# Performance work log

Measured on AMD Instinct MI355X. Metric: run time of the kernel, lower is better.

Reference implementation:

```python
import jax, jax.numpy as jnp
import numpy as np
from jax import lax

K = 3      # kernel_size
C = 64     # n_feat
B, H, W = 2, 256, 256


def _conv(x, w, b, pad):
    # NCHW conv, stride 1
    out = lax.conv_general_dilated(x, w, (1, 1), [(pad, pad), (pad, pad)],
                                   dimension_numbers=('NCHW', 'OIHW', 'NCHW'))
    return out + b[None, :, None, None]


def _prelu(x, a):
    # nn.PReLU() with a single shared learnable slope (init 0.25)
    return jnp.where(x >= 0, x, a * x)


def setup_inputs():
    key = jax.random.key(0)
    ks = jax.random.split(key, 20)
    s = 0.05
    def w(k, shape):
        return jax.random.normal(k, shape, jnp.float32) * s
    inp = {
        'image': jax.random.normal(ks[0], (B, C, H, W), jnp.float32),
        'guidance': jax.random.normal(ks[1], (B, C, H, W), jnp.float32),
        # self.tensor: 1x1 conv (2C -> C) + PReLU (shared with jbf_conv's act)
        'tensor_w': w(ks[2], (C, 2 * C, 1, 1)),
        'tensor_b': jnp.zeros((C,), jnp.float32),
        'a_jbf': jnp.full((1,), 0.25, jnp.float32),
        'kg_w1': w(ks[3], (C, C, 3, 3)), 'kg_b1': jnp.zeros((C,), jnp.float32),
        'kg_w2': w(ks[4], (C, C, 3, 3)), 'kg_b2': jnp.zeros((C,), jnp.float32),
        'kg_w3': w(ks[5], (C, C, 3, 3)), 'kg_b3': jnp.zeros((C,), jnp.float32),
        'kg_w4': w(ks[6], (C, C, 3, 3)), 'kg_b4': jnp.zeros((C,), jnp.float32),
        'kg_w5': w(ks[7], (K * K * C, C, 1, 1)),
        'kg_b5': jnp.zeros((K * K * C,), jnp.float32),
        'a_kg': jnp.full((1,), 0.25, jnp.float32),
        # jbf_conv: 3x3 C->C, PReLU (shared a_jbf), 3x3 C->C
        'jbf_w1': w(ks[8], (C, C, 3, 3)), 'jbf_b1': jnp.zeros((C,), jnp.float32),
        'jbf_w2': w(ks[9], (C, C, 3, 3)), 'jbf_b2': jnp.zeros((C,), jnp.float32),
    }
    return inp


def reference(image, guidance, tensor_w, tensor_b, a_jbf,
              kg_w1, kg_b1, kg_w2, kg_b2, kg_w3, kg_b3, kg_w4, kg_b4,
              kg_w5, kg_b5, a_kg, jbf_w1, jbf_b1, jbf_w2, jbf_b2):
    b, c, h, w = image.shape
    # fuse target+guidance features
    t = _prelu(_conv(jnp.concatenate([image, guidance], axis=1), tensor_w, tensor_b, 0), a_jbf)
    # concat_kg: predict per-pixel dynamic kernel (b, K*K*c, h, w)
    y = t
    for wt, bs in ((kg_w1, kg_b1), (kg_w2, kg_b2), (kg_w3, kg_b3), (kg_w4, kg_b4)):
        y = _prelu(_conv(y, wt, bs, 1), a_kg)
    bi_kernel = _conv(y, kg_w5, kg_b5, 0)
    # unfold: torch layout is channel-major (c, ki, kj) along dim 1
    p = (K - 1) // 2
    xp = jnp.pad(image, ((0, 0), (0, 0), (p, p), (p, p)))
    taps = [xp[:, :, i:i + h, j:j + w] for i in range(K) for j in range(K)]
    patch = jnp.stack(taps, axis=2).reshape(b, c * K * K, h, w)
    # NOTE: faithful to source -- (c*K*K) flat layout reinterpreted as (K*K, c)
    jbf = (patch * bi_kernel).reshape(b, K * K, c, h, w).sum(axis=1)
    out = _conv(_prelu(_conv(jbf, jbf_w1, jbf_b1, 1), a_jbf), jbf_w2, jbf_b2, 1)
    return out + image
```

## Files before the change

### kernel.cpp

```cpp
#include <hip/hip_runtime.h>

#define HW 65536

typedef __bf16 bf16x8 __attribute__((ext_vector_type(8)));
typedef float f32x16 __attribute__((ext_vector_type(16)));

__device__ inline unsigned short f2bf(float x) {
    union { float f; unsigned u; } v; v.f = x;
    unsigned r = v.u + 0x7FFF + ((v.u >> 16) & 1);
    return (unsigned short)(r >> 16);
}
__device__ inline float bfhi2f(unsigned u) {
    union { unsigned u; float f; } v; v.u = u & 0xffff0000u; return v.f;
}
__device__ inline float bflo2f(unsigned u) {
    union { unsigned u; float f; } v; v.u = u << 16; return v.f;
}

union FragU { uint4 u; bf16x8 v; };
__device__ inline bf16x8 ld_frag(const uint4* p) { FragU t; t.u = *p; return t.v; }

__global__ __launch_bounds__(256) void k_wprep(
    const float* __restrict__ w0, const float* __restrict__ w1,
    const float* __restrict__ w2, const float* __restrict__ w3,
    const float* __restrict__ w4, const float* __restrict__ w5,
    const float* __restrict__ w5c, const float* __restrict__ tw,
    unsigned short* __restrict__ wT)
{
    int y = blockIdx.y;
    unsigned short* o = wT + (size_t)y * 36864;
    if (y < 6) {
        const float* ws_[6] = {w0, w1, w2, w3, w4, w5};
        const float* w = ws_[y];
        for (int e = blockIdx.x * 256 + threadIdx.x; e < 36864; e += gridDim.x * 256) {
            int tap = e >> 12, oc = (e >> 6) & 63, ic = e & 63;
            int h = ic >> 5, ig = (ic >> 3) & 3, j = ic & 7;
            int dst = ((h * 2304) + (tap * 4 + ig) * 64 + oc) * 8 + j;
            o[dst] = f2bf(w[(oc * 64 + ic) * 9 + tap]);
        }
    } else if (y == 6) {
        for (int e = blockIdx.x * 256 + threadIdx.x; e < 36864; e += gridDim.x * 256)
            o[e] = f2bf(w5c[e]);
    } else {
        for (int e = blockIdx.x * 256 + threadIdx.x; e < 8192; e += gridDim.x * 256) {
            int oc = e >> 7, ic = e & 127;
            int kg = ic >> 3, j = ic & 7;
            o[((kg * 64 + oc) << 3) + j] = f2bf(tw[e]);
        }
    }
}

__global__ __launch_bounds__(256) void k_tr(
    const float* __restrict__ img, const float* __restrict__ gd,
    unsigned short* __restrict__ imgT, unsigned short* __restrict__ gdT)
{
    __shared__ float sT[64 * 66];
    int tid = threadIdx.x;
    int z = blockIdx.y;
    int b = z & 1;
    const float* src = (z >> 1) ? gd : img;
    unsigned short* dst = (z >> 1) ? gdT : imgT;
    int px0 = blockIdx.x * 64;
    size_t sbase = (size_t)b * 64 * HW + px0;

#pragma unroll
    for (int i = 0; i < 4; ++i) {
        int e = i * 256 + tid;
        int ic = e >> 4, seg = e & 15;
        float4 v = *(const float4*)(src + sbase + (size_t)ic * HW + seg * 4);
        float* p = &sT[ic * 66 + seg * 4];
        ((float2*)p)[0] = make_float2(v.x, v.y);
        ((float2*)p)[1] = make_float2(v.z, v.w);
    }
    __syncthreads();

    size_t dbase = (size_t)b * HW * 64 + (size_t)px0 * 64;
#pragma unroll
    for (int k = 0; k < 2; ++k) {
        int idx = k * 256 + tid;
        int px = idx >> 3, u = idx & 7;
        union { uint4 q; unsigned short h[8]; } o;
#pragma unroll
        for (int j = 0; j < 8; ++j)
            o.h[j] = f2bf(sT[(u * 8 + j) * 66 + px]);
        *(uint4*)(dst + dbase + (size_t)px * 64 + u * 8) = o.q;
    }
}

__global__ __launch_bounds__(256, 4) void k_fusem(
    const unsigned short* __restrict__ imgT, const unsigned short* __restrict__ gdT,
    const unsigned short* __restrict__ wTf, const float* __restrict__ bias,
    const float* __restrict__ a, unsigned short* __restrict__ out)
{
    __shared__ __align__(16) char smem[18688];
    uint4* sX = (uint4*)smem;
    float* sB = (float*)(smem + 18432);
    unsigned short* sT16 = (unsigned short*)smem;

    int tid = threadIdx.x;
    int wv = tid >> 6, lane = tid & 63;
    int half = lane >> 5, l31 = lane & 31;
    int b = blockIdx.z;
    int y0 = blockIdx.y * 8, x0 = blockIdx.x * 16;
    size_t zbase = (size_t)b * HW * 64;
    const uint4* wg = (const uint4*)wTf;

    if (tid < 64) sB[tid] = bias[tid];

    f32x16 acc[2];
#pragma unroll
    for (int i = 0; i < 2; ++i)
#pragma unroll
        for (int r = 0; r < 16; ++r) acc[i][r] = 0.f;

    auto loadX = [&](const unsigned short* src, uint4* rx) {
#pragma unroll
        for (int i = 0; i < 4; ++i) {
            int e = i * 256 + tid;
            int px = e >> 3, ig = e & 7;
            int gy = y0 + (px >> 4), gx = x0 + (px & 15);
            rx[i] = *(const uint4*)(src + zbase + ((size_t)(gy * 256 + gx)) * 64 + ig * 8);
        }
    };
    auto writeX = [&](const uint4* rx) {
#pragma unroll
        for (int i = 0; i < 4; ++i) {
            int e = i * 256 + tid;
            sX[(e >> 3) * 9 + (e & 7)] = rx[i];
        }
    };
    auto compute = [&](int h) {
#pragma unroll
        for (int c = 0; c < 4; ++c) {
            int ig = c * 2 + half;
            int kg = h * 8 + ig;
            bf16x8 a0 = ld_frag(&wg[kg * 64 + l31]);
            bf16x8 a1 = ld_frag(&wg[kg * 64 + 32 + l31]);
            int p0 = wv * 32 + l31;
            bf16x8 b0 = ld_frag(&sX[p0 * 9 + ig]);
            acc[0] = __builtin_amdgcn_mfma_f32_32x32x16_bf16(a0, b0, acc[0], 0, 0, 0);
            acc[1] = __builtin_amdgcn_mfma_f32_32x32x16_bf16(a1, b0, acc[1], 0, 0, 0);
        }
    };

    uint4 rx[4], ry[4];
    loadX(imgT, rx);
    writeX(rx);
    loadX(gdT, ry);
    __syncthreads();
    compute(0);
    __syncthreads();
    writeX(ry);
    __syncthreads();
    compute(1);

    float slope = a[0];
    __syncthreads();
    {
        int px = wv * 32 + l31;
#pragma unroll
        for (int ot = 0; ot < 2; ++ot)
#pragma unroll
            for (int q2 = 0; q2 < 4; ++q2) {
                unsigned short hw[4];
#pragma unroll
                for (int j = 0; j < 4; ++j) {
                    int r = (q2 << 2) | j;
                    int oc = ot * 32 + j + 8 * q2 + 4 * half;
                    float v = acc[ot][r] + sB[oc];
                    v = (v >= 0.f) ? v : slope * v;
                    hw[j] = f2bf(v);
                }
                int unit = ot * 4 + q2;
                int up = unit ^ (px & 7);
                uint2* p = (uint2*)&sT16[px * 64 + up * 8 + half * 4];
                *p = make_uint2((unsigned)hw[0] | ((unsigned)hw[1] << 16),
                                (unsigned)hw[2] | ((unsigned)hw[3] << 16));
            }
    }
    __syncthreads();
#pragma unroll
    for (int k = 0; k < 4; ++k) {
        int idx = k * 256 + tid;
        int row = idx >> 7, rem = idx & 127;
        int col = rem >> 3, u = rem & 7;
        int px = row * 16 + col;
        uint4 v = *(uint4*)&sT16[px * 64 + (u ^ (px & 7)) * 8];
        *(uint4*)(out + zbase + ((size_t)((y0 + row) * 256 + x0 + col)) * 64 + u * 8) = v;
    }
}

#define XU 5

template<int MODE>
__global__ __launch_bounds__(256, 4) void k_conv3m(
    const unsigned short* __restrict__ in, const unsigned short* __restrict__ wT,
    const float* __restrict__ bias, const float* __restrict__ a,
    const float* __restrict__ res, void* __restrict__ outv)
{
    __shared__ __align__(16) char smem[29312];
    uint4* sX0 = (uint4*)smem;
    uint4* sX1 = (uint4*)(smem + 14400);
    float* sB = (float*)(smem + 28800);
    unsigned short* sT16 = (unsigned short*)smem;

    int tid = threadIdx.x;
    int wv = tid >> 6, lane = tid & 63;
    int half = lane >> 5, l31 = lane & 31;
    int b = blockIdx.z;
    int y0 = blockIdx.y * 8, x0 = blockIdx.x * 16;
    const size_t zbase = (size_t)b * HW * 64;
    const uint4* wg = (const uint4*)wT;

    if (tid < 64) sB[tid] = bias[tid];

    f32x16 acc[2];
#pragma unroll
    for (int i = 0; i < 2; ++i)
#pragma unroll
        for (int r = 0; r < 16; ++r) acc[i][r] = 0.f;

    auto loadX = [&](int h, uint4* rx) {
#pragma unroll
        for (int i = 0; i < 3; ++i) {
            int e = i * 256 + tid;
            int cell = e >> 2, ig = e & 3;
            int r = cell / 18, c2 = cell - r * 18;
            int gy = y0 + r - 1, gx = x0 + c2 - 1;
            rx[i] = make_uint4(0, 0, 0, 0);
            if (e < 720 && gy >= 0 && gy < 256 && gx >= 0 && gx < 256)
                rx[i] = *(const uint4*)(in + zbase + ((size_t)(gy * 256 + gx)) * 64 + h * 32 + ig * 8);
        }
    };
    auto writeX = [&](uint4* sXd, const uint4* rx) {
#pragma unroll
        for (int i = 0; i < 3; ++i) {
            int e = i * 256 + tid;
            if (e < 720) sXd[(e >> 2) * XU + (e & 3)] = rx[i];
        }
    };
    auto compute = [&](int h, const uint4* sXp) {
#pragma unroll
        for (int tap = 0; tap < 9; ++tap) {
            int dy = tap / 3, dx = tap % 3;
#pragma unroll
            for (int c = 0; c < 2; ++c) {
                int ig = c * 2 + half;
                bf16x8 a0 = ld_frag(&wg[h * 2304 + (tap * 4 + ig) * 64 + l31]);
                bf16x8 a1 = ld_frag(&wg[h * 2304 + (tap * 4 + ig) * 64 + 32 + l31]);
                int p0 = wv * 32 + l31;
                int u0 = ((((p0 >> 4) + dy) * 18) + (p0 & 15) + dx) * XU + ig;
                bf16x8 b0 = ld_frag(&sXp[u0]);
                acc[0] = __builtin_amdgcn_mfma_f32_32x32x16_bf16(a0, b0, acc[0], 0, 0, 0);
                acc[1] = __builtin_amdgcn_mfma_f32_32x32x16_bf16(a1, b0, acc[1], 0, 0, 0);
            }
        }
    };

    uint4 rx[3];
    loadX(0, rx);
    writeX(sX0, rx);
    __syncthreads();
    loadX(1, rx);
    compute(0, sX0);
    writeX(sX1, rx);
    __syncthreads();
    compute(1, sX1);

    if (MODE == 0) {
        float slope = a[0];
        __syncthreads();
        {
            int px = wv * 32 + l31;
#pragma unroll
            for (int ot = 0; ot < 2; ++ot)
#pragma unroll
                for (int q2 = 0; q2 < 4; ++q2) {
                    unsigned short hw[4];
#pragma unroll
                    for (int j = 0; j < 4; ++j) {
                        int r = (q2 << 2) | j;
                        int oc = ot * 32 + j + 8 * q2 + 4 * half;
                        float v = acc[ot][r] + sB[oc];
                        v = (v >= 0.f) ? v : slope * v;
                        hw[j] = f2bf(v);
                    }
                    int unit = ot * 4 + q2;
                    int up = unit ^ (px & 7);
                    uint2* p = (uint2*)&sT16[px * 64 + up * 8 + half * 4];
                    *p = make_uint2((unsigned)hw[0] | ((unsigned)hw[1] << 16),
                                    (unsigned)hw[2] | ((unsigned)hw[3] << 16));
                }
        }
        __syncthreads();
        unsigned short* outT = (unsigned short*)outv;
#pragma unroll
        for (int k = 0; k < 4; ++k) {
            int idx = k * 256 + tid;
            int row = idx >> 7, rem = idx & 127;
            int col = rem >> 3, u = rem & 7;
            int px = row * 16 + col;
            uint4 v = *(uint4*)&sT16[px * 64 + (u ^ (px & 7)) * 8];
            *(uint4*)(outT + zbase + ((size_t)((y0 + row) * 256 + x0 + col)) * 64 + u * 8) = v;
        }
    } else {
        float* outF = (float*)outv;
        int p = wv * 32 + l31;
        int y = y0 + (p >> 4), x = x0 + (p & 15);
        size_t pbase = (size_t)b * 64 * HW + (size_t)y * 256 + x;
#pragma unroll
        for (int ot = 0; ot < 2; ++ot)
#pragma unroll
            for (int r = 0; r < 16; ++r) {
                int oc = ot * 32 + (r & 3) + 8 * (r >> 2) + 4 * half;
                float v = acc[ot][r] + sB[oc];
                v += res[pbase + (size_t)oc * HW];
                outF[pbase + (size_t)oc * HW] = v;
            }
    }
}

struct OffTab { unsigned v[9][32]; int chlo[9]; };
constexpr OffTab make_tab() {
    OffTab t{};
    for (int kk = 0; kk < 9; ++kk) {
        int chlo = (kk * 64) / 9;
        t.chlo[kk] = chlo;
        for (int ot = 0; ot < 2; ++ot)
            for (int r = 0; r < 16; ++r) {
                int cc0 = ot * 32 + (r & 3) + 8 * (r >> 2);
                int q0 = kk * 64 + cc0, q1 = q0 + 4;
                int o0 = (q0 / 9 - chlo) * 360 + (q0 % 9 / 3) * 40 + (q0 % 9 % 3);
                int o1 = (q1 / 9 - chlo) * 360 + (q1 % 9 / 3) * 40 + (q1 % 9 % 3);
                t.v[kk][ot * 16 + r] = (unsigned)o0 | ((unsigned)o1 << 16);
            }
    }
    return t;
}
__constant__ OffTab kOff = make_tab();

__global__ __launch_bounds__(256, 2) void k_jbfm(
    const unsigned short* __restrict__ y4, const float* __restrict__ img,
    const unsigned short* __restrict__ w5T, const float* __restrict__ b5,
    unsigned short* __restrict__ out)
{
    __shared__ __align__(16) char smem[78592];
    uint4* sY = (uint4*)smem;
    float* sB5 = (float*)(smem + 76288);
    unsigned short* sT16 = (unsigned short*)smem;

    int tid = threadIdx.x;
    int wv = tid >> 6, lane = tid & 63;
    int half = lane >> 5, l31 = lane & 31;
    int b = blockIdx.z;
    int y0 = blockIdx.y * 8, x0 = blockIdx.x * 32;
    size_t zbase = (size_t)b * HW * 64;
    size_t ibase = (size_t)b * 64 * HW;

    int p_off[3], p_dst[3];
    bool p_a[3], p_b[3], p_act[3];
#pragma unroll
    for (int i = 0; i < 3; ++i) {
        int e = i * 256 + tid;
        bool act = e < 720;
        int ch = e / 90, rem = e - ch * 90;
        int rp = rem / 10, seg = rem - rp * 10;
        int gy = y0 + rp - 1;
        int gxb = x0 - 4 + seg * 4;
        bool xok = (gxb >= 0 && gxb < 256);
        p_act[i] = act;
        p_a[i] = act && xok && gy >= 0 && gy < 256;
        p_b[i] = act && xok && (gy + 1) < 256;
        p_off[i] = ch * HW + gy * 256 + gxb;
        p_dst[i] = ch * 360 + rp * 40 + seg * 4;
    }

#pragma unroll
    for (int i = 0; i < 8; ++i) {
        int e = i * 256 + tid;
        int px = e >> 3, ig = e & 7;
        int gy = y0 + (px >> 5), gx = x0 + (px & 31);
        sY[px * 9 + ig] = *(const uint4*)(y4 + zbase + ((size_t)(gy * 256 + gx)) * 64 + ig * 8);
    }
    for (int e = tid; e < 576; e += 256) sB5[e] = b5[e];

    {
        uint4* sW50 = (uint4*)(smem + 36864);
        unsigned* sP0 = (unsigned*)(smem + 53248);
#pragma unroll
        for (int u = 0; u < 2; ++u) {
            int uu = u * 256 + tid;
            int cc = uu & 63, ig = uu >> 6;
            sW50[uu] = ((const uint4*)w5T)[cc * 8 + ig];
        }
        const float* rp0 = img + ibase;
#pragma unroll
        for (int i = 0; i < 3; ++i) {
            float4 fa = make_float4(0, 0, 0, 0), fb = make_float4(0, 0, 0, 0);
            if (p_a[i]) fa = *(const float4*)(rp0 + p_off[i]);
            if (p_b[i]) fb = *(const float4*)(rp0 + p_off[i] + 256);
            if (p_act[i]) {
                uint4 pk;
                pk.x = (unsigned)f2bf(fa.x) | ((unsigned)f2bf(fb.x) << 16);
                pk.y = (unsigned)f2bf(fa.y) | ((unsigned)f2bf(fb.y) << 16);
                pk.z = (unsigned)f2bf(fa.z) | ((unsigned)f2bf(fb.z) << 16);
                pk.w = (unsigned)f2bf(fa.w) | ((unsigned)f2bf(fb.w) << 16);
                *(uint4*)&sP0[p_dst[i]] = pk;
            }
        }
    }

    float jb[2][2][16];
#pragma unroll
    for (int i = 0; i < 2; ++i)
#pragma unroll
        for (int j = 0; j < 2; ++j)
#pragma unroll
            for (int r = 0; r < 16; ++r) jb[i][j][r] = 0.f;

    __syncthreads();

#pragma unroll 1
    for (int kk = 0; kk < 9; ++kk) {
        const int cur = kk & 1;
        const uint4* sW5c = (const uint4*)(smem + 36864 + cur * 8192);
        const unsigned* sPc = (const unsigned*)(smem + 53248 + cur * 11520);

        uint4 wpre0, wpre1;
        float4 pfa[3], pfb[3];
        if (kk < 8) {
            const int nk = kk + 1;
            const int chlo_n = kOff.chlo[nk];
            {
                int cc = tid & 63, ig = tid >> 6;
                wpre0 = ((const uint4*)w5T)[(nk * 64 + cc) * 8 + ig];
                int uu = 256 + tid;
                int cc1 = uu & 63, ig1 = uu >> 6;
                wpre1 = ((const uint4*)w5T)[(nk * 64 + cc1) * 8 + ig1];
            }
            const float* rp0 = img + ibase + (size_t)chlo_n * HW;
#pragma unroll
            for (int i = 0; i < 3; ++i) {
                pfa[i] = make_float4(0, 0, 0, 0);
                pfb[i] = make_float4(0, 0, 0, 0);
                if (p_a[i]) pfa[i] = *(const float4*)(rp0 + p_off[i]);
                if (p_b[i]) pfb[i] = *(const float4*)(rp0 + p_off[i] + 256);
            }
        }

        f32x16 acc[2][2];
#pragma unroll
        for (int ot = 0; ot < 2; ++ot)
#pragma unroll
            for (int r = 0; r < 16; ++r) {
                int cc0 = ot * 32 + (r & 3) + 8 * (r >> 2);
                float bv = sB5[kk * 64 + cc0 + 4 * half];
                acc[ot][0][r] = bv;
                acc[ot][1][r] = bv;
            }

#pragma unroll
        for (int c = 0; c < 4; ++c) {
            int ig = c * 2 + half;
            bf16x8 a0 = ld_frag(&sW5c[ig * 64 + l31]);
            bf16x8 a1 = ld_frag(&sW5c[ig * 64 + 32 + l31]);
            int p0 = wv * 64 + l31;
            bf16x8 b0 = ld_frag(&sY[p0 * 9 + ig]);
            bf16x8 b1 = ld_frag(&sY[(p0 + 32) * 9 + ig]);
            acc[0][0] = __builtin_amdgcn_mfma_f32_32x32x16_bf16(a0, b0, acc[0][0], 0, 0, 0);
            acc[0][1] = __builtin_amdgcn_mfma_f32_32x32x16_bf16(a0, b1, acc[0][1], 0, 0, 0);
            acc[1][0] = __builtin_amdgcn_mfma_f32_32x32x16_bf16(a1, b0, acc[1][0], 0, 0, 0);
            acc[1][1] = __builtin_amdgcn_mfma_f32_32x32x16_bf16(a1, b1, acc[1][1], 0, 0, 0);
        }

        {
            const unsigned* basep = sPc + wv * 80 + l31 + 3;
            const unsigned* tab = kOff.v[kk];
#pragma unroll
            for (int ot = 0; ot < 2; ++ot)
#pragma unroll
                for (int r = 0; r < 16; ++r) {
                    unsigned oo = tab[ot * 16 + r];
                    unsigned o0 = oo & 0xffffu, o1 = oo >> 16;
                    unsigned pv = basep[half ? o1 : o0];
                    jb[ot][0][r] = fmaf(acc[ot][0][r], bflo2f(pv), jb[ot][0][r]);
                    jb[ot][1][r] = fmaf(acc[ot][1][r], bfhi2f(pv), jb[ot][1][r]);
                }
        }

        if (kk < 8) {
            uint4* sW5n = (uint4*)(smem + 36864 + (cur ^ 1) * 8192);
            unsigned* sPn = (unsigned*)(smem + 53248 + (cur ^ 1) * 11520);
            sW5n[tid] = wpre0;
            sW5n[256 + tid] = wpre1;
#pragma unroll
            for (int i = 0; i < 3; ++i) {
                if (p_act[i]) {
                    uint4 pk;
                    pk.x = (unsigned)f2bf(pfa[i].x) | ((unsigned)f2bf(pfb[i].x) << 16);
                    pk.y = (unsigned)f2bf(pfa[i].y) | ((unsigned)f2bf(pfb[i].y) << 16);
                    pk.z = (unsigned)f2bf(pfa[i].z) | ((unsigned)f2bf(pfb[i].z) << 16);
                    pk.w = (unsigned)f2bf(pfa[i].w) | ((unsigned)f2bf(pfb[i].w) << 16);
                    *(uint4*)&sPn[p_dst[i]] = pk;
                }
            }
        }
        __syncthreads();
    }

#pragma unroll
    for (int ot = 0; ot < 2; ++ot)
#pragma unroll
        for (int pt = 0; pt < 2; ++pt) {
            int px = wv * 64 + pt * 32 + l31;
#pragma unroll
            for (int q2 = 0; q2 < 4; ++q2) {
                unsigned short hw[4];
#pragma unroll
                for (int j = 0; j < 4; ++j) {
                    int r = (q2 << 2) | j;
                    hw[j] = f2bf(jb[ot][pt][r]);
                }
                int unit = ot * 4 + q2;
                int up = unit ^ (px & 7);
                uint2* p = (uint2*)&sT16[px * 64 + up * 8 + half * 4];
                *p = make_uint2((unsigned)hw[0] | ((unsigned)hw[1] << 16),
                                (unsigned)hw[2] | ((unsigned)hw[3] << 16));
            }
        }
    __syncthreads();
#pragma unroll
    for (int k = 0; k < 8; ++k) {
        int col = tid >> 3, u = tid & 7;
        int px = k * 32 + col;
        uint4 v = *(uint4*)&sT16[px * 64 + (u ^ (px & 7)) * 8];
        *(uint4*)(out + zbase + ((size_t)((y0 + k) * 256 + x0 + col)) * 64 + u * 8) = v;
    }
}

extern "C" void kernel_launch(void* const* d_in, const int* in_sizes, int n_in,
                              void* d_out, int out_size, void* d_ws, size_t ws_size,
                              hipStream_t stream) {
    const float* img  = (const float*)d_in[0];
    const float* gd   = (const float*)d_in[1];
    const float* tw   = (const float*)d_in[2];
    const float* tb   = (const float*)d_in[3];
    const float* ajbf = (const float*)d_in[4];
    const float* kw1  = (const float*)d_in[5];
    const float* kb1  = (const float*)d_in[6];
    const float* kw2  = (const float*)d_in[7];
    const float* kb2  = (const float*)d_in[8];
    const float* kw3  = (const float*)d_in[9];
    const float* kb3  = (const float*)d_in[10];
    const float* kw4  = (const float*)d_in[11];
    const float* kb4  = (const float*)d_in[12];
    const float* kw5  = (const float*)d_in[13];
    const float* kb5  = (const float*)d_in[14];
    const float* akg  = (const float*)d_in[15];
    const float* jw1  = (const float*)d_in[16];
    const float* jb1  = (const float*)d_in[17];
    const float* jw2  = (const float*)d_in[18];
    const float* jb2  = (const float*)d_in[19];
    float* out  = (float*)d_out;

    const size_t TEN = (size_t)2 * HW * 64;
    unsigned short* bufA = (unsigned short*)d_ws;
    unsigned short* imgT = bufA + TEN;
    unsigned short* gdT  = imgT + TEN;
    unsigned short* wT   = gdT + TEN;
    unsigned short* bufB = (unsigned short*)d_out;

    dim3 gs(16, 32, 2);
    dim3 gw(8, 32, 2);

    k_tr<<<dim3(1024, 4), 256, 0, stream>>>(img, gd, imgT, gdT);
    k_wprep<<<dim3(4, 8), 256, 0, stream>>>(kw1, kw2, kw3, kw4, jw1, jw2, kw5, tw, wT);

    k_fusem<<<gs, 256, 0, stream>>>(imgT, gdT, wT + (size_t)7 * 36864, tb, ajbf, bufA);

    k_conv3m<0><<<gs, 256, 0, stream>>>(bufA, wT + (size_t)0 * 36864, kb1, akg, nullptr, bufB);
    k_conv3m<0><<<gs, 256, 0, stream>>>(bufB, wT + (size_t)1 * 36864, kb2, akg, nullptr, bufA);
    k_conv3m<0><<<gs, 256, 0, stream>>>(bufA, wT + (size_t)2 * 36864, kb3, akg, nullptr, bufB);
    k_conv3m<0><<<gs, 256, 0, stream>>>(bufB, wT + (size_t)3 * 36864, kb4, akg, nullptr, bufA);

    k_jbfm<<<gw, 256, 0, stream>>>(bufA, img, wT + (size_t)6 * 36864, kb5, bufB);

    k_conv3m<0><<<gs, 256, 0, stream>>>(bufB, wT + (size_t)4 * 36864, jb1, ajbf, nullptr, bufA);
    k_conv3m<2><<<gs, 256, 0, stream>>>(bufA, wT + (size_t)5 * 36864, jb2, ajbf, img, out);
}
```

Measured before the change: 313.1 us.

## Fuse consecutive 3x3 conv pairs into one kernel with halo recompute

Replaces the single 3x3 conv kernel with one that runs two chained 3x3 convs per tile. It loads a 20x12 input halo, computes the intermediate 18x10 activation into shared memory (zeroed outside the image), then runs the second conv from shared memory. This removes three kernel launches and the global round trips of the intermediate activations. In exchange it recomputes halo pixels, which adds about 40% extra MFMA work in the first conv, uses more shared memory, and splits the work unevenly because only two of the four waves handle the extra cells. The weight layout is also changed to an interleaved tap-major order.

After: 314.3 us. About the same (+0.4%).

```diff
diff --git a/kernel.cpp b/kernel.cpp
--- a/kernel.cpp
+++ b/kernel.cpp
@@ -34,8 +34,8 @@
         const float* w = ws_[y];
         for (int e = blockIdx.x * 256 + threadIdx.x; e < 36864; e += gridDim.x * 256) {
             int tap = e >> 12, oc = (e >> 6) & 63, ic = e & 63;
-            int h = ic >> 5, ig = (ic >> 3) & 3, j = ic & 7;
-            int dst = ((h * 2304) + (tap * 4 + ig) * 64 + oc) * 8 + j;
+            int igg = ic >> 3, j = ic & 7;
+            int dst = ((tap * 8 + igg) * 64 + oc) * 8 + j;
             o[dst] = f2bf(w[(oc * 64 + ic) * 9 + tap]);
         }
     } else if (y == 6) {
@@ -193,16 +193,17 @@
 #define XU 5
 
 template<int MODE>
-__global__ __launch_bounds__(256, 4) void k_conv3m(
-    const unsigned short* __restrict__ in, const unsigned short* __restrict__ wT,
-    const float* __restrict__ bias, const float* __restrict__ a,
-    const float* __restrict__ res, void* __restrict__ outv)
+__global__ __launch_bounds__(256, 4) void k_conv2x(
+    const unsigned short* __restrict__ in,
+    const unsigned short* __restrict__ w1T, const unsigned short* __restrict__ w2T,
+    const float* __restrict__ b1, const float* __restrict__ b2,
+    const float* __restrict__ a, const float* __restrict__ res,
+    void* __restrict__ outv)
 {
-    __shared__ __align__(16) char smem[29312];
-    uint4* sX0 = (uint4*)smem;
-    uint4* sX1 = (uint4*)(smem + 14400);
-    float* sB = (float*)(smem + 28800);
-    unsigned short* sT16 = (unsigned short*)smem;
+    __shared__ __align__(16) char smem[38912];
+    uint4* sIn0 = (uint4*)smem;
+    uint4* sIn1 = (uint4*)(smem + 19200);
+    float* sB = (float*)(smem + 38400);
 
     int tid = threadIdx.x;
     int wv = tid >> 6, lane = tid & 63;
@@ -210,68 +211,94 @@
     int b = blockIdx.z;
     int y0 = blockIdx.y * 8, x0 = blockIdx.x * 16;
     const size_t zbase = (size_t)b * HW * 64;
-    const uint4* wg = (const uint4*)wT;
-
-    if (tid < 64) sB[tid] = bias[tid];
-
-    f32x16 acc[2];
-#pragma unroll
-    for (int i = 0; i < 2; ++i)
-#pragma unroll
-        for (int r = 0; r < 16; ++r) acc[i][r] = 0.f;
-
-    auto loadX = [&](int h, uint4* rx) {
-#pragma unroll
-        for (int i = 0; i < 3; ++i) {
+    const uint4* wg1 = (const uint4*)w1T;
+    const uint4* wg2 = (const uint4*)w2T;
+
+    if (tid < 64) sB[tid] = b1[tid];
+    else if (tid < 128) sB[tid] = b2[tid - 64];
+
+    auto loadIn = [&](int h, uint4* rx) {
+#pragma unroll
+        for (int i = 0; i < 4; ++i) {
             int e = i * 256 + tid;
             int cell = e >> 2, ig = e & 3;
-            int r = cell / 18, c2 = cell - r * 18;
-            int gy = y0 + r - 1, gx = x0 + c2 - 1;
+            int r = cell / 20, c2 = cell - r * 20;
+            int gy = y0 - 2 + r, gx = x0 - 2 + c2;
             rx[i] = make_uint4(0, 0, 0, 0);
-            if (e < 720 && gy >= 0 && gy < 256 && gx >= 0 && gx < 256)
+            if (e < 960 && gy >= 0 && gy < 256 && gx >= 0 && gx < 256)
                 rx[i] = *(const uint4*)(in + zbase + ((size_t)(gy * 256 + gx)) * 64 + h * 32 + ig * 8);
         }
     };
-    auto writeX = [&](uint4* sXd, const uint4* rx) {
-#pragma unroll
-        for (int i = 0; i < 3; ++i) {
+    auto writeIn = [&](uint4* s, const uint4* rx) {
+#pragma unroll
+        for (int i = 0; i < 4; ++i) {
             int e = i * 256 + tid;
-            if (e < 720) sXd[(e >> 2) * XU + (e & 3)] = rx[i];
+            if (e < 960) s[(e >> 2) * XU + (e & 3)] = rx[i];
         }
     };
-    auto compute = [&](int h, const uint4* sXp) {
-#pragma unroll
-        for (int tap = 0; tap < 9; ++tap) {
-            int dy = tap / 3, dx = tap % 3;
-#pragma unroll
-            for (int c = 0; c < 2; ++c) {
-                int ig = c * 2 + half;
-                bf16x8 a0 = ld_frag(&wg[h * 2304 + (tap * 4 + ig) * 64 + l31]);
-                bf16x8 a1 = ld_frag(&wg[h * 2304 + (tap * 4 + ig) * 64 + 32 + l31]);
-                int p0 = wv * 32 + l31;
-                int u0 = ((((p0 >> 4) + dy) * 18) + (p0 & 15) + dx) * XU + ig;
-                bf16x8 b0 = ld_frag(&sXp[u0]);
-                acc[0] = __builtin_amdgcn_mfma_f32_32x32x16_bf16(a0, b0, acc[0], 0, 0, 0);
-                acc[1] = __builtin_amdgcn_mfma_f32_32x32x16_bf16(a1, b0, acc[1], 0, 0, 0);
+
+    const bool two = (wv < 2);
+    int cell0 = wv * 32 + l31;
+    int ib0 = (cell0 / 18) * 20 + (cell0 % 18);
+    int cell1 = (wv + 4) * 32 + l31;
+    int cc1 = cell1 < 179 ? cell1 : 179;
+    int ib1 = (cc1 / 18) * 20 + (cc1 % 18);
+
+    f32x16 acc1[2][2];
+#pragma unroll
+    for (int s = 0; s < 2; ++s)
+#pragma unroll
+        for (int i = 0; i < 2; ++i)
+#pragma unroll
+            for (int r = 0; r < 16; ++r) acc1[s][i][r] = 0.f;
+
+    auto conv1_h = [&](int h, const uint4* sInp) {
+#pragma unroll 1
+        for (int dy = 0; dy < 3; ++dy) {
+#pragma unroll
+            for (int dx = 0; dx < 3; ++dx) {
+                int tap = dy * 3 + dx;
+                int doff = dy * 20 + dx;
+#pragma unroll
+                for (int c = 0; c < 2; ++c) {
+                    int ig = c * 2 + half;
+                    bf16x8 a0 = ld_frag(&wg1[(tap * 8 + h * 4 + ig) * 64 + l31]);
+                    bf16x8 a1 = ld_frag(&wg1[(tap * 8 + h * 4 + ig) * 64 + 32 + l31]);
+                    bf16x8 bb0 = ld_frag(&sInp[(ib0 + doff) * XU + ig]);
+                    acc1[0][0] = __builtin_amdgcn_mfma_f32_32x32x16_bf16(a0, bb0, acc1[0][0], 0, 0, 0);
+                    acc1[0][1] = __builtin_amdgcn_mfma_f32_32x32x16_bf16(a1, bb0, acc1[0][1], 0, 0, 0);
+                    if (two) {
+                        bf16x8 bb1 = ld_frag(&sInp[(ib1 + doff) * XU + ig]);
+                        acc1[1][0] = __builtin_amdgcn_mfma_f32_32x32x16_bf16(a0, bb1, acc1[1][0], 0, 0, 0);
+                        acc1[1][1] = __builtin_amdgcn_mfma_f32_32x32x16_bf16(a1, bb1, acc1[1][1], 0, 0, 0);
+                    }
+                }
             }
         }
     };
 
-    uint4 rx[3];
-    loadX(0, rx);
-    writeX(sX0, rx);
-    __syncthreads();
-    loadX(1, rx);
-    compute(0, sX0);
-    writeX(sX1, rx);
-    __syncthreads();
-    compute(1, sX1);
-
-    if (MODE == 0) {
-        float slope = a[0];
-        __syncthreads();
-        {
-            int px = wv * 32 + l31;
+    uint4 rx[4];
+    loadIn(0, rx);
+    writeIn(sIn0, rx);
+    uint4 ry[4];
+    loadIn(1, ry);
+    __syncthreads();
+    conv1_h(0, sIn0);
+    writeIn(sIn1, ry);
+    __syncthreads();
+    conv1_h(1, sIn1);
+
+    float s1 = a[0];
+    __syncthreads();
+    unsigned short* sC16 = (unsigned short*)smem;
+#pragma unroll
+    for (int s = 0; s < 2; ++s) {
+        if (s == 1 && !two) break;
+        int cell = (wv + s * 4) * 32 + l31;
+        if (cell < 180) {
+            int orow = cell / 18, ocol = cell - orow * 18;
+            int gy = y0 - 1 + orow, gx = x0 - 1 + ocol;
+            bool inb = (gy >= 0 && gy < 256 && gx >= 0 && gx < 256);
 #pragma unroll
             for (int ot = 0; ot < 2; ++ot)
 #pragma unroll
@@ -281,8 +308,66 @@
                     for (int j = 0; j < 4; ++j) {
                         int r = (q2 << 2) | j;
                         int oc = ot * 32 + j + 8 * q2 + 4 * half;
-                        float v = acc[ot][r] + sB[oc];
-                        v = (v >= 0.f) ? v : slope * v;
+                        float v = acc1[s][ot][r] + sB[oc];
+                        v = (v >= 0.f) ? v : s1 * v;
+                        if (!inb) v = 0.f;
+                        hw[j] = f2bf(v);
+                    }
+                    int up = (ot * 4 + q2) ^ (cell & 7);
+                    *(uint2*)&sC16[cell * 64 + up * 8 + half * 4] =
+                        make_uint2((unsigned)hw[0] | ((unsigned)hw[1] << 16),
+                                   (unsigned)hw[2] | ((unsigned)hw[3] << 16));
+                }
+        }
+    }
+    __syncthreads();
+
+    f32x16 acc2[2];
+#pragma unroll
+    for (int i = 0; i < 2; ++i)
+#pragma unroll
+        for (int r = 0; r < 16; ++r) acc2[i][r] = 0.f;
+
+    {
+        int p0 = wv * 32 + l31;
+        int row = p0 >> 4, col = p0 & 15;
+        const uint4* sC4 = (const uint4*)smem;
+#pragma unroll 1
+        for (int dy = 0; dy < 3; ++dy) {
+#pragma unroll
+            for (int dx = 0; dx < 3; ++dx) {
+                int tap = dy * 3 + dx;
+                int cl = (row + dy) * 18 + col + dx;
+                int cb = cl * 8, sx = cl & 7;
+#pragma unroll
+                for (int c = 0; c < 4; ++c) {
+                    int ig = c * 2 + half;
+                    bf16x8 a0 = ld_frag(&wg2[(tap * 8 + ig) * 64 + l31]);
+                    bf16x8 a1 = ld_frag(&wg2[(tap * 8 + ig) * 64 + 32 + l31]);
+                    bf16x8 bb = ld_frag(&sC4[cb + (ig ^ sx)]);
+                    acc2[0] = __builtin_amdgcn_mfma_f32_32x32x16_bf16(a0, bb, acc2[0], 0, 0, 0);
+                    acc2[1] = __builtin_amdgcn_mfma_f32_32x32x16_bf16(a1, bb, acc2[1], 0, 0, 0);
+                }
+            }
+        }
+    }
+
+    if (MODE == 0) {
+        __syncthreads();
+        unsigned short* sT16 = (unsigned short*)smem;
+        {
+            int px = wv * 32 + l31;
+#pragma unroll
+            for (int ot = 0; ot < 2; ++ot)
+#pragma unroll
+                for (int q2 = 0; q2 < 4; ++q2) {
+                    unsigned short hw[4];
+#pragma unroll
+                    for (int j = 0; j < 4; ++j) {
+                        int r = (q2 << 2) | j;
+                        int oc = ot * 32 + j + 8 * q2 + 4 * half;
+                        float v = acc2[ot][r] + sB[64 + oc];
+                        v = (v >= 0.f) ? v : s1 * v;
                         hw[j] = f2bf(v);
                     }
                     int unit = ot * 4 + q2;
@@ -313,7 +398,7 @@
 #pragma unroll
             for (int r = 0; r < 16; ++r) {
                 int oc = ot * 32 + (r & 3) + 8 * (r >> 2) + 4 * half;
-                float v = acc[ot][r] + sB[oc];
+                float v = acc2[ot][r] + sB[64 + oc];
                 v += res[pbase + (size_t)oc * HW];
                 outF[pbase + (size_t)oc * HW] = v;
             }
@@ -569,6 +654,7 @@
     unsigned short* gdT  = imgT + TEN;
     unsigned short* wT   = gdT + TEN;
     unsigned short* bufB = (unsigned short*)d_out;
+    unsigned short* bufC = gdT;
 
     dim3 gs(16, 32, 2);
     dim3 gw(8, 32, 2);
@@ -578,13 +664,13 @@
 
     k_fusem<<<gs, 256, 0, stream>>>(imgT, gdT, wT + (size_t)7 * 36864, tb, ajbf, bufA);
 
-    k_conv3m<0><<<gs, 256, 0, stream>>>(bufA, wT + (size_t)0 * 36864, kb1, akg, nullptr, bufB);
-    k_conv3m<0><<<gs, 256, 0, stream>>>(bufB, wT + (size_t)1 * 36864, kb2, akg, nullptr, bufA);
-    k_conv3m<0><<<gs, 256, 0, stream>>>(bufA, wT + (size_t)2 * 36864, kb3, akg, nullptr, bufB);
-    k_conv3m<0><<<gs, 256, 0, stream>>>(bufB, wT + (size_t)3 * 36864, kb4, akg, nullptr, bufA);
-
-    k_jbfm<<<gw, 256, 0, stream>>>(bufA, img, wT + (size_t)6 * 36864, kb5, bufB);
-
-    k_conv3m<0><<<gs, 256, 0, stream>>>(bufB, wT + (size_t)4 * 36864, jb1, ajbf, nullptr, bufA);
-    k_conv3m<2><<<gs, 256, 0, stream>>>(bufA, wT + (size_t)5 * 36864, jb2, ajbf, img, out);
-}
+    k_conv2x<0><<<gs, 256, 0, stream>>>(bufA, wT + (size_t)0 * 36864, wT + (size_t)1 * 36864,
+                                        kb1, kb2, akg, nullptr, bufB);
+    k_conv2x<0><<<gs, 256, 0, stream>>>(bufB, wT + (size_t)2 * 36864, wT + (size_t)3 * 36864,
+                                        kb3, kb4, akg, nullptr, bufA);
+
+    k_jbfm<<<gw, 256, 0, stream>>>(bufA, img, wT + (size_t)6 * 36864, kb5, bufC);
+
+    k_conv2x<2><<<gs, 256, 0, stream>>>(bufC, wT + (size_t)4 * 36864, wT + (size_t)5 * 36864,
+                                        jb1, jb2, ajbf, img, out);
+}
```
